# Kernel tuning notes

Hardware: AMD Instinct MI355X
Metric: run time of the kernel (lower is better)

Reference implementation:

```python
import jax, jax.numpy as jnp
import numpy as np

B, N, RESC, LAT, UNIT = 8, 32, 256.0, 1536, 512
CHS = [64, 64, 128, 256, 512, 512]
HS = [128, 64, 32, 16, 8, 1]


def _align(feat, P):
    # torch F.grid_sample(feat, 2*P.unsqueeze(-2)/RESC - 1, 'bilinear', 'border', align_corners=False).squeeze(-1)
    # feat: [B,C,H,W], P: [B,M,2] (x,y) pixel coords in [0,RESC); returns [B,C,M]
    Bn, C, H, W = feat.shape
    gx = 2.0 * P[..., 0] / RESC - 1.0
    gy = 2.0 * P[..., 1] / RESC - 1.0
    # align_corners=False unnormalize, then border clamp
    x = jnp.clip(((gx + 1.0) * W - 1.0) * 0.5, 0.0, W - 1.0)
    y = jnp.clip(((gy + 1.0) * H - 1.0) * 0.5, 0.0, H - 1.0)
    x0 = jnp.floor(x); y0 = jnp.floor(y)
    wx = (x - x0)[:, None, :]; wy = (y - y0)[:, None, :]
    x0i = x0.astype(jnp.int32); y0i = y0.astype(jnp.int32)
    x1i = jnp.minimum(x0i + 1, W - 1); y1i = jnp.minimum(y0i + 1, H - 1)
    flat = feat.reshape(Bn, C, H * W)
    def gat(yi, xi):
        return jnp.take_along_axis(flat, (yi * W + xi)[:, None, :], axis=2)  # [B,C,M]
    v00 = gat(y0i, x0i); v01 = gat(y0i, x1i); v10 = gat(y1i, x0i); v11 = gat(y1i, x1i)
    return v00 * (1 - wx) * (1 - wy) + v01 * wx * (1 - wy) + v10 * (1 - wx) * wy + v11 * wx * wy


def _conv1(x, w, b):
    # 1x1 Conv1d: [B,Cin,M] x [Cout,Cin] -> [B,Cout,M]
    return jnp.einsum('bci,oc->boi', x, w) + b[None, :, None]


def _rescls(x, p):
    # ResCls(n=1): intro -> (relu(BN) -> chorus, residual) -> outro ; BN in eval mode
    iw, ib, bg, bb, bm, bv, cw, cb, ow, ob = p
    x = _conv1(x, iw, ib)
    d = jax.nn.relu((x - bm[None, :, None]) * (bg / jnp.sqrt(bv + 1e-5))[None, :, None] + bb[None, :, None])
    x = x + _conv1(d, cw, cb)
    return _conv1(x, ow, ob)


def _forward(feats, P, n, gp, pp):
    # node features: concat of per-level aligned features  [B, LAT, N]
    F_ = jnp.concatenate([_align(f, P) for f in feats], axis=1)
    # edge midpoints ep[b, i*N+j] = (P[i] + P[j]) / 2  -> [B, N*N, 2]
    ep = ((P[:, :, None, :] + P[:, None, :, :]) * 0.5).reshape(B, N * N, 2)
    # L: first LAT channels = F[:, :, i], next LAT channels = F[:, :, j]
    Fi = jnp.broadcast_to(F_[:, :, :, None], (B, LAT, N, N)).reshape(B, LAT, N * N)
    Fj = jnp.broadcast_to(F_[:, :, None, :], (B, LAT, N, N)).reshape(B, LAT, N * N)
    E = jnp.concatenate([_align(f, ep) for f in feats], axis=1)  # [B, LAT, N*N]
    CE = jnp.concatenate([Fi, Fj, E], axis=1)  # [B, 3*LAT, N*N]
    gate = jax.nn.sigmoid(_rescls(CE, gp))  # [B, 1, N*N]
    pr = _rescls(CE, pp)  # [B, 64, N*N]
    pr = pr / jnp.maximum(jnp.linalg.norm(pr, axis=1, keepdims=True), 1e-12)  # F.normalize(dim=1)
    m = jnp.arange(N) < n[:, None]  # [B, N]
    mask = (m[:, None, :] & m[:, :, None]).reshape(B, 1, N * N).astype(CE.dtype)
    return (gate * pr * mask).reshape(B, 64, N, N)


def setup_inputs() -> dict:
    key = jax.random.key(0)
    ks = jax.random.split(key, 20)
    d = {}
    for i, (c, h) in enumerate(zip(CHS, HS)):
        d[f'feat{i}'] = jax.random.normal(ks[i], (B, c, h, h), jnp.float32)
    d['P'] = jax.random.uniform(ks[6], (B, N, 2), jnp.float32) * RESC
    d['n'] = jax.random.randint(ks[7], (B,), 16, N + 1, jnp.int32)
    def w(k, shape):
        return jax.random.normal(k, shape, jnp.float32) * 0.02
    for pre, cout, k0 in (('g', 1, 8), ('p', 64, 12)):
        d[pre + '_iw'] = w(ks[k0], (UNIT, 3 * LAT)); d[pre + '_ib'] = jnp.zeros((UNIT,), jnp.float32)
        d[pre + '_bg'] = jnp.ones((UNIT,), jnp.float32); d[pre + '_bb'] = jnp.zeros((UNIT,), jnp.float32)
        d[pre + '_bm'] = jnp.zeros((UNIT,), jnp.float32)
        d[pre + '_bv'] = jax.random.uniform(ks[k0 + 1], (UNIT,), jnp.float32) + 0.5
        d[pre + '_cw'] = w(ks[k0 + 2], (UNIT, UNIT)); d[pre + '_cb'] = jnp.zeros((UNIT,), jnp.float32)
        d[pre + '_ow'] = w(ks[k0 + 3], (cout, UNIT)); d[pre + '_ob'] = jnp.zeros((cout,), jnp.float32)
    return d


def reference(feat0, feat1, feat2, feat3, feat4, feat5, P, n,
              g_iw, g_ib, g_bg, g_bb, g_bm, g_bv, g_cw, g_cb, g_ow, g_ob,
              p_iw, p_ib, p_bg, p_bb, p_bm, p_bv, p_cw, p_cb, p_ow, p_ob):
    feats = (feat0, feat1, feat2, feat3, feat4, feat5)
    gp = (g_iw, g_ib, g_bg, g_bb, g_bm, g_bv, g_cw, g_cb, g_ow, g_ob)
    pp = (p_iw, p_ib, p_bg, p_bb, p_bm, p_bv, p_cw, p_cb, p_ow, p_ob)
    return _forward(feats, P, n, gp, pp)
```

## Files before the change

kernel.cpp:

```cpp
#include <hip/hip_runtime.h>
#include <hip/hip_bf16.h>

using bf16 = __hip_bfloat16;
using short8 = __attribute__((ext_vector_type(8))) short;
using f32x4  = __attribute__((ext_vector_type(4))) float;
typedef unsigned int u32;

#define LAT_ 1536

__device__ __forceinline__ void glds16(const bf16* g, bf16* l) {
  __builtin_amdgcn_global_load_lds(
      (const __attribute__((address_space(1))) void*)g,
      (__attribute__((address_space(3))) void*)l, 16, 0, 0);
}
__device__ __forceinline__ float b2f(bf16 x) { return __bfloat162float(x); }
__device__ __forceinline__ bf16 f2b(float x) { return __float2bfloat16(x); }

template<int C, int W>
__device__ __forceinline__ void trans_tile(const float* __restrict__ src, bf16* __restrict__ dst,
                                           int b, int hw0, int c0, bf16 (*tile)[72], int t) {
  constexpr int HW = W * W;
  {
    int cl = t >> 2, h0 = (t & 3) * 16;
    const float* sp = src + (long)(b * C + c0 + cl) * HW + hw0 + h0;
    #pragma unroll
    for (int k = 0; k < 16; k += 4) {
      float4 v = *(const float4*)(sp + k);
      tile[h0 + k + 0][cl] = f2b(v.x);
      tile[h0 + k + 1][cl] = f2b(v.y);
      tile[h0 + k + 2][cl] = f2b(v.z);
      tile[h0 + k + 3][cl] = f2b(v.w);
    }
  }
  __syncthreads();
  {
    int hwl = t >> 2, cc = (t & 3) * 16;
    bf16* dp = dst + ((long)b * HW + hw0 + hwl) * C + c0 + cc;
    #pragma unroll
    for (int k = 0; k < 16; k += 2) {
      __hip_bfloat162 pr;
      pr.x = tile[hwl][cc + k];
      pr.y = tile[hwl][cc + k + 1];
      *(__hip_bfloat162*)(dp + k) = pr;
    }
  }
}

__global__ __launch_bounds__(256) void prep_k(
    const float* __restrict__ g_iw, const float* __restrict__ p_iw,
    const float* __restrict__ p_cw, const float* __restrict__ p_ow, const float* __restrict__ f5,
    const float* __restrict__ g_bg, const float* __restrict__ g_bb, const float* __restrict__ g_bm,
    const float* __restrict__ g_bv, const float* __restrict__ p_bg, const float* __restrict__ p_bb,
    const float* __restrict__ p_bm, const float* __restrict__ p_bv,
    const float* __restrict__ g_ib, const float* __restrict__ p_ib, const float* __restrict__ p_cb,
    const float* __restrict__ g_ow, const float* __restrict__ g_cw,
    const float* __restrict__ g_cb, const float* __restrict__ g_ob,
    const float* __restrict__ f0, const float* __restrict__ f1, const float* __restrict__ f2,
    const float* __restrict__ f3, const float* __restrict__ f4,
    bf16* __restrict__ Wp, bf16* __restrict__ pcw16, bf16* __restrict__ pow16,
    bf16* __restrict__ T5, float* __restrict__ bnp, float* __restrict__ u,
    float* __restrict__ gacc,
    bf16* __restrict__ T0, bf16* __restrict__ T1, bf16* __restrict__ T2,
    bf16* __restrict__ T3, bf16* __restrict__ T4) {
  __shared__ bf16 tile[64][72];
  __shared__ float red[256];
  int B = blockIdx.x, t = threadIdx.x;
  if (B < 18432) {
    int seg = B / 3072;
    int idx = (B % 3072) * 256 + t;
    if (idx < 512 * 1536) {
      int r = idx / 1536, c = idx % 1536;
      const float* src; int co;
      switch (seg) {
        case 0: src = g_iw; co = 0;    break;
        case 1: src = g_iw; co = 1536; break;
        case 2: src = p_iw; co = 0;    break;
        case 3: src = p_iw; co = 1536; break;
        case 4: src = g_iw; co = 3072; break;
        default: src = p_iw; co = 3072; break;
      }
      Wp[(long)seg * 512 * 1536 + idx] = f2b(src[(long)r * 4608 + co + c]);
    }
    return;
  }
  if (B < 19456) { int idx = (B - 18432) * 256 + t; pcw16[idx] = f2b(p_cw[idx]); return; }
  if (B < 19584) { int idx = (B - 19456) * 256 + t; pow16[idx] = f2b(p_ow[idx]); return; }
  if (B < 19600) { int idx = (B - 19584) * 256 + t; T5[idx] = f2b(f5[idx]); return; }
  if (B < 19602) {
    int k = (B - 19600) * 256 + t;
    if (k < 512) {
      float sg = g_bg[k] / sqrtf(g_bv[k] + 1e-5f);
      bnp[k] = sg; bnp[512 + k] = g_bb[k] - g_bm[k] * sg;
      float sp = p_bg[k] / sqrtf(p_bv[k] + 1e-5f);
      bnp[1024 + k] = sp; bnp[1536 + k] = p_bb[k] - p_bm[k] * sp;
      bnp[2048 + k] = g_ib[k]; bnp[2560 + k] = p_ib[k];
      bnp[3584 + k] = p_cb[k];
    }
    return;
  }
  if (B < 19610) {
    __shared__ float ured[4][64];
    int k0 = (B - 19602) * 64;
    int kk = t & 63, part = t >> 6;
    int k = k0 + kk;
    float s = 0.f;
    for (int o = part * 128; o < part * 128 + 128; ++o)
      s = fmaf(g_ow[o], g_cw[o * 512 + k], s);
    ured[part][kk] = s;
    __syncthreads();
    if (part == 0) u[k] = ured[0][kk] + ured[1][kk] + ured[2][kk] + ured[3][kk];
    return;
  }
  if (B == 19610) {
    red[t] = g_ow[t] * g_cb[t] + g_ow[t + 256] * g_cb[t + 256];
    __syncthreads();
    for (int off = 128; off; off >>= 1) {
      if (t < off) red[t] += red[t + off];
      __syncthreads();
    }
    if (t == 0) bnp[3072] = red[0] + g_ob[0];
    return;
  }
  if (B < 19643) { int idx = (B - 19611) * 256 + t; gacc[idx] = 0.f; return; }
  {
    int q = B - 19643;
    int b = q / 376, tt = q % 376;
    if (tt < 256)      trans_tile<64, 128>(f0, T0, b, tt * 64, 0, tile, t);
    else if (tt < 320) trans_tile<64, 64 >(f1, T1, b, (tt - 256) * 64, 0, tile, t);
    else if (tt < 352) { int z = tt - 320; trans_tile<128, 32>(f2, T2, b, (z & 15) * 64, (z >> 4) * 64, tile, t); }
    else if (tt < 368) { int z = tt - 352; trans_tile<256, 16>(f3, T3, b, (z & 3) * 64, (z >> 2) * 64, tile, t); }
    else               { int z = tt - 368; trans_tile<512, 8 >(f4, T4, b, 0, z * 64, tile, t); }
  }
}

__device__ __forceinline__ float blo(u32 r) { return __uint_as_float(r << 16); }
__device__ __forceinline__ float bhi(u32 r) { return __uint_as_float(r & 0xffff0000u); }

template<int C, int W>
__device__ __forceinline__ void proc2(const bf16* __restrict__ T, int b,
    const float* MX, const float* MY, bf16* __restrict__ Sb, int koff, int t) {
  constexpr int C2 = C / 2, HW = W * W;
  const bf16* Tb = T + (long)b * HW * C;
  for (int idx = t; idx < 16 * C2; idx += 256) {
    int q = idx / C2, c2 = idx % C2;
    float x = MX[q], y = MY[q];
    float fx = fminf(fmaxf(x * ((float)W / 256.f) - 0.5f, 0.f), (float)(W - 1));
    float fy = fminf(fmaxf(y * ((float)W / 256.f) - 0.5f, 0.f), (float)(W - 1));
    float x0f = floorf(fx), y0f = floorf(fy);
    float wx = fx - x0f, wy = fy - y0f;
    int x0 = (int)x0f, y0 = (int)y0f;
    int x1 = min(x0 + 1, W - 1), y1 = min(y0 + 1, W - 1);
    u32 r00 = *(const u32*)&Tb[(y0 * W + x0) * C + 2 * c2];
    u32 r01 = *(const u32*)&Tb[(y0 * W + x1) * C + 2 * c2];
    u32 r10 = *(const u32*)&Tb[(y1 * W + x0) * C + 2 * c2];
    u32 r11 = *(const u32*)&Tb[(y1 * W + x1) * C + 2 * c2];
    float w00 = (1.f - wx) * (1.f - wy), w01 = wx * (1.f - wy);
    float w10 = (1.f - wx) * wy,        w11 = wx * wy;
    float vlo = blo(r00) * w00 + blo(r01) * w01 + blo(r10) * w10 + blo(r11) * w11;
    float vhi = bhi(r00) * w00 + bhi(r01) * w01 + bhi(r10) * w10 + bhi(r11) * w11;
    __hip_bfloat162 pr;
    pr.x = f2b(vlo); pr.y = f2b(vhi);
    *(__hip_bfloat162*)&Sb[(long)q * LAT_ + koff + 2 * c2] = pr;
  }
}

__global__ __launch_bounds__(256) void sample5_k(
    const bf16* __restrict__ T0, const bf16* __restrict__ T1, const bf16* __restrict__ T2,
    const bf16* __restrict__ T3, const bf16* __restrict__ T4, const bf16* __restrict__ T5,
    const float* __restrict__ P, bf16* __restrict__ Sball) {
  int b = blockIdx.z, p0 = blockIdx.x * 16, lvl = blockIdx.y, t = threadIdx.x;
  __shared__ float Px[32], Py[32], MX[16], MY[16];
  if (t < 32) { Px[t] = P[(b * 32 + t) * 2]; Py[t] = P[(b * 32 + t) * 2 + 1]; }
  __syncthreads();
  if (t < 16) {
    int m = p0 + t;
    float x, y;
    if (m < 32) { x = Px[m]; y = Py[m]; }
    else { int ij = m - 32, i = ij >> 5, j = ij & 31;
           x = 0.5f * (Px[i] + Px[j]); y = 0.5f * (Py[i] + Py[j]); }
    MX[t] = x; MY[t] = y;
  }
  __syncthreads();
  bf16* Sb = Sball + ((long)b * 1056 + p0) * LAT_;
  switch (lvl) {
    case 0: proc2<64, 128>(T0, b, MX, MY, Sb, 0,    t); break;
    case 1: proc2<64, 64 >(T1, b, MX, MY, Sb, 64,   t); break;
    case 2: proc2<128, 32>(T2, b, MX, MY, Sb, 128,  t); break;
    case 3: proc2<256, 16>(T3, b, MX, MY, Sb, 256,  t); break;
    case 4: proc2<512, 8 >(T4, b, MX, MY, Sb, 512,  t); break;
    default:
      for (int idx = t; idx < 16 * 256; idx += 256) {
        int q = idx >> 8, c2 = idx & 255;
        *(__hip_bfloat162*)&Sb[(long)q * LAT_ + 1024 + 2 * c2] =
            *(const __hip_bfloat162*)&T5[b * 512 + 2 * c2];
      }
  }
}

__global__ __launch_bounds__(256) void nodegemm_k(
    const bf16* __restrict__ Sball, const bf16* __restrict__ Wp, float* __restrict__ A4) {
  int b = blockIdx.y;
  int n0 = blockIdx.x * 64;
  int t = threadIdx.x, w = t >> 6, lane = t & 63;
  int nn = n0 + w * 16;
  int frow = lane & 15, fko = (lane >> 4) * 8;
  const bf16* Ab = Sball + (long)b * 1056 * LAT_;
  f32x4 acc[2] = {};
  for (int kb = 0; kb < LAT_; kb += 32) {
    short8 bq = *(const short8*)&Wp[(long)(nn + frow) * LAT_ + kb + fko];
    #pragma unroll
    for (int i = 0; i < 2; ++i) {
      short8 aq = *(const short8*)&Ab[(long)(i * 16 + frow) * LAT_ + kb + fko];
      acc[i] = __builtin_amdgcn_mfma_f32_16x16x32_bf16(aq, bq, acc[i], 0, 0, 0);
    }
  }
  #pragma unroll
  for (int i = 0; i < 2; ++i)
    #pragma unroll
    for (int r = 0; r < 4; ++r) {
      int m = i * 16 + (lane >> 4) * 4 + r;
      int n = nn + (lane & 15);
      A4[(long)b * 65536 + m * 2048 + n] = acc[i][r];
    }
}

__global__ __launch_bounds__(256) void edge_k(
    const bf16* __restrict__ Sball, const bf16* __restrict__ WpE,
    const float* __restrict__ bnp, const float* __restrict__ A4,
    const float* __restrict__ u, const float* __restrict__ g_ow,
    bf16* __restrict__ XFh, bf16* __restrict__ DH, float* __restrict__ gacc) {
  int b = blockIdx.z;
  int m0 = blockIdx.x * 128, n0 = blockIdx.y * 128;
  const bf16* A = Sball + (long)b * 1056 * LAT_ + 32 * LAT_;
  __shared__ bf16 Ash[128 * 32];
  __shared__ bf16 Bsh[128 * 32];
  int t = threadIdx.x, w = t >> 6, lane = t & 63;
  int mh = (w & 1) * 64, nh = (w >> 1) * 64;
  int frow = lane & 15, fko = (lane >> 4) * 8;
  int lrow = lane >> 2, lchunk = lane & 3;
  f32x4 acc[4][4] = {};
  for (int kb = 0; kb < LAT_; kb += 32) {
    #pragma unroll
    for (int q = 0; q < 2; ++q) {
      int ra = q * 64 + w * 16 + lrow;
      glds16(&A[(long)(m0 + ra) * LAT_ + kb + lchunk * 8],   &Ash[ra * 32 + lchunk * 8]);
      glds16(&WpE[(long)(n0 + ra) * LAT_ + kb + lchunk * 8], &Bsh[ra * 32 + lchunk * 8]);
    }
    __syncthreads();
    short8 af[4], bq[4];
    #pragma unroll
    for (int i = 0; i < 4; ++i) af[i] = *(const short8*)&Ash[(mh + i * 16 + frow) * 32 + fko];
    #pragma unroll
    for (int j = 0; j < 4; ++j) bq[j] = *(const short8*)&Bsh[(nh + j * 16 + frow) * 32 + fko];
    #pragma unroll
    for (int i = 0; i < 4; ++i)
      #pragma unroll
      for (int j = 0; j < 4; ++j)
        acc[i][j] = __builtin_amdgcn_mfma_f32_16x16x32_bf16(af[i], bq[j], acc[i][j], 0, 0, 0);
    __syncthreads();
  }
  if (n0 < 512) {
    float pg[16];
    #pragma unroll
    for (int z = 0; z < 16; ++z) pg[z] = 0.f;
    #pragma unroll
    for (int i = 0; i < 4; ++i) {
      #pragma unroll
      for (int j = 0; j < 4; ++j) {
        int n = n0 + nh + j * 16 + (lane & 15);
        float gw = g_ow[n], uu = u[n];
        float sc = bnp[n], sh = bnp[512 + n], ib = bnp[2048 + n];
        #pragma unroll
        for (int r = 0; r < 4; ++r) {
          int m = m0 + mh + i * 16 + (lane >> 4) * 4 + r;
          float v = acc[i][j][r] + ib
                  + A4[((long)b * 32 + (m >> 5)) * 2048 + n]
                  + A4[((long)b * 32 + (m & 31)) * 2048 + 512 + n];
          float d = fmaxf(fmaf(v, sc, sh), 0.f);
          pg[i * 4 + r] += gw * v + uu * d;
        }
      }
    }
    #pragma unroll
    for (int z = 0; z < 16; ++z) {
      float v = pg[z];
      v += __shfl_xor(v, 1, 16);
      v += __shfl_xor(v, 2, 16);
      v += __shfl_xor(v, 4, 16);
      v += __shfl_xor(v, 8, 16);
      pg[z] = v;
    }
    if ((lane & 15) == 0) {
      #pragma unroll
      for (int z = 0; z < 16; ++z) {
        int m = m0 + mh + (z >> 2) * 16 + (lane >> 4) * 4 + (z & 3);
        atomicAdd(&gacc[(long)b * 1024 + m], pg[z]);
      }
    }
  } else {
    #pragma unroll
    for (int i = 0; i < 4; ++i) {
      #pragma unroll
      for (int j = 0; j < 4; ++j) {
        int n = n0 + nh + j * 16 + (lane & 15);
        int np = n - 512;
        float sc = bnp[1024 + np], sh = bnp[1536 + np], ib = bnp[2048 + n];
        #pragma unroll
        for (int r = 0; r < 4; ++r) {
          int m = m0 + mh + i * 16 + (lane >> 4) * 4 + r;
          float v = acc[i][j][r] + ib
                  + A4[((long)b * 32 + (m >> 5)) * 2048 + 1024 + np]
                  + A4[((long)b * 32 + (m & 31)) * 2048 + 1536 + np];
          long e = ((long)b * 1024 + m) * 512 + np;
          XFh[e] = f2b(v);
          DH[e]  = f2b(fmaxf(fmaf(v, sc, sh), 0.f));
        }
      }
    }
  }
}

__global__ __launch_bounds__(256) void chorus_k(
    const bf16* __restrict__ DH, const bf16* __restrict__ pcw16,
    const float* __restrict__ bnp, const bf16* __restrict__ XFh,
    bf16* __restrict__ Yp16) {
  int b = blockIdx.z;
  int m0 = blockIdx.x * 128, n0 = blockIdx.y * 128;
  const bf16* A = DH + (long)b * 1024 * 512;
  __shared__ bf16 Ash[128 * 32];
  __shared__ bf16 Bsh[128 * 32];
  int t = threadIdx.x, w = t >> 6, lane = t & 63;
  int mh = (w & 1) * 64, nh = (w >> 1) * 64;
  int frow = lane & 15, fko = (lane >> 4) * 8;
  int lrow = lane >> 2, lchunk = lane & 3;
  f32x4 acc[4][4] = {};
  for (int kb = 0; kb < 512; kb += 32) {
    #pragma unroll
    for (int q = 0; q < 2; ++q) {
      int ra = q * 64 + w * 16 + lrow;
      glds16(&A[(long)(m0 + ra) * 512 + kb + lchunk * 8],      &Ash[ra * 32 + lchunk * 8]);
      glds16(&pcw16[(long)(n0 + ra) * 512 + kb + lchunk * 8],  &Bsh[ra * 32 + lchunk * 8]);
    }
    __syncthreads();
    short8 af[4], bq[4];
    #pragma unroll
    for (int i = 0; i < 4; ++i) af[i] = *(const short8*)&Ash[(mh + i * 16 + frow) * 32 + fko];
    #pragma unroll
    for (int j = 0; j < 4; ++j) bq[j] = *(const short8*)&Bsh[(nh + j * 16 + frow) * 32 + fko];
    #pragma unroll
    for (int i = 0; i < 4; ++i)
      #pragma unroll
      for (int j = 0; j < 4; ++j)
        acc[i][j] = __builtin_amdgcn_mfma_f32_16x16x32_bf16(af[i], bq[j], acc[i][j], 0, 0, 0);
    __syncthreads();
  }
  #pragma unroll
  for (int i = 0; i < 4; ++i)
    #pragma unroll
    for (int j = 0; j < 4; ++j)
      #pragma unroll
      for (int r = 0; r < 4; ++r) {
        int m = m0 + mh + i * 16 + (lane >> 4) * 4 + r;
        int n = n0 + nh + j * 16 + (lane & 15);
        float v = acc[i][j][r] + bnp[3584 + n]
                + b2f(XFh[((long)b * 1024 + m) * 512 + n]);
        Yp16[((long)b * 1024 + m) * 512 + n] = f2b(v);
      }
}

__global__ __launch_bounds__(256) void ofinal_k(
    const bf16* __restrict__ Yp16, const bf16* __restrict__ pow16,
    const float* __restrict__ p_ob, const float* __restrict__ gacc,
    const float* __restrict__ bnp, const int* __restrict__ nvec,
    float* __restrict__ out) {
  int b = blockIdx.y;
  int m0 = blockIdx.x * 64;
  const bf16* Ab = Yp16 + (long)b * 1024 * 512;
  __shared__ bf16 Ash[64][40];
  __shared__ bf16 Bsh[64][40];
  __shared__ float ol[64][65];
  int t = threadIdx.x, w = t >> 6, lane = t & 63;
  int mq = w * 16;
  int frow = lane & 15, fko = (lane >> 4) * 8;
  f32x4 acc[4] = {};
  for (int kb = 0; kb < 512; kb += 32) {
    { int r = t >> 2, ko = (t & 3) * 8;
      *(uint4*)&Ash[r][ko] = *(const uint4*)&Ab[(long)(m0 + r) * 512 + kb + ko];
      *(uint4*)&Bsh[r][ko] = *(const uint4*)&pow16[(long)r * 512 + kb + ko]; }
    __syncthreads();
    short8 af = *(const short8*)&Ash[mq + frow][fko];
    #pragma unroll
    for (int j = 0; j < 4; ++j) {
      short8 bq = *(const short8*)&Bsh[j * 16 + frow][fko];
      acc[j] = __builtin_amdgcn_mfma_f32_16x16x32_bf16(af, bq, acc[j], 0, 0, 0);
    }
    __syncthreads();
  }
  float pr[4][4], ssl[4] = {0.f, 0.f, 0.f, 0.f};
  #pragma unroll
  for (int j = 0; j < 4; ++j) {
    float bias = p_ob[j * 16 + (lane & 15)];
    #pragma unroll
    for (int r = 0; r < 4; ++r) {
      float v = acc[j][r] + bias;
      pr[j][r] = v;
      ssl[r] = fmaf(v, v, ssl[r]);
    }
  }
  #pragma unroll
  for (int r = 0; r < 4; ++r) {
    float v = ssl[r];
    v += __shfl_xor(v, 1, 16);
    v += __shfl_xor(v, 2, 16);
    v += __shfl_xor(v, 4, 16);
    v += __shfl_xor(v, 8, 16);
    ssl[r] = v;
  }
  int nb = nvec[b];
  float gconst = bnp[3072];
  float scale[4];
  #pragma unroll
  for (int r = 0; r < 4; ++r) {
    int m = m0 + mq + (lane >> 4) * 4 + r;
    float gl = gacc[(long)b * 1024 + m] + gconst;
    float gate = 1.f / (1.f + expf(-gl));
    int ii = m >> 5, jj = m & 31;
    float maskv = (ii < nb && jj < nb) ? 1.f : 0.f;
    scale[r] = gate * maskv / fmaxf(sqrtf(ssl[r]), 1e-12f);
  }
  #pragma unroll
  for (int j = 0; j < 4; ++j)
    #pragma unroll
    for (int r = 0; r < 4; ++r)
      ol[mq + (lane >> 4) * 4 + r][j * 16 + (lane & 15)] = pr[j][r] * scale[r];
  __syncthreads();
  {
    int c = t >> 2, ms = (t & 3) * 16;
    float* op = out + ((long)b * 64 + c) * 1024 + m0 + ms;
    #pragma unroll
    for (int k = 0; k < 16; k += 4) {
      float4 v;
      v.x = ol[ms + k + 0][c];
      v.y = ol[ms + k + 1][c];
      v.z = ol[ms + k + 2][c];
      v.w = ol[ms + k + 3][c];
      *(float4*)(op + k) = v;
    }
  }
}

extern "C" void kernel_launch(void* const* d_in, const int* in_sizes, int n_in,
                              void* d_out, int out_size, void* d_ws, size_t ws_size,
                              hipStream_t stream) {
  const float* f0 = (const float*)d_in[0];
  const float* f1 = (const float*)d_in[1];
  const float* f2 = (const float*)d_in[2];
  const float* f3 = (const float*)d_in[3];
  const float* f4 = (const float*)d_in[4];
  const float* f5 = (const float*)d_in[5];
  const float* P  = (const float*)d_in[6];
  const int*   n  = (const int*)d_in[7];
  const float *g_iw=(const float*)d_in[8],  *g_ib=(const float*)d_in[9],
              *g_bg=(const float*)d_in[10], *g_bb=(const float*)d_in[11],
              *g_bm=(const float*)d_in[12], *g_bv=(const float*)d_in[13],
              *g_cw=(const float*)d_in[14], *g_cb=(const float*)d_in[15],
              *g_ow=(const float*)d_in[16], *g_ob=(const float*)d_in[17];
  const float *p_iw=(const float*)d_in[18], *p_ib=(const float*)d_in[19],
              *p_bg=(const float*)d_in[20], *p_bb=(const float*)d_in[21],
              *p_bm=(const float*)d_in[22], *p_bv=(const float*)d_in[23],
              *p_cw=(const float*)d_in[24], *p_cb=(const float*)d_in[25],
              *p_ow=(const float*)d_in[26], *p_ob=(const float*)d_in[27];
  float* out = (float*)d_out;
  char* wsb = (char*)d_ws;

  bf16*  Sb    = (bf16*)(wsb + 0);
  bf16*  Wp    = (bf16*)(wsb + 25952256);
  bf16*  pcw16 = (bf16*)(wsb + 35389440);
  bf16*  pow16 = (bf16*)(wsb + 35913728);
  bf16*  T5    = (bf16*)(wsb + 35979264);
  float* bnp   = (float*)(wsb + 35987456);
  float* u     = (float*)(wsb + 36003840);
  float* gacc  = (float*)(wsb + 36005888);
  float* A4    = (float*)(wsb + 36038656);
  bf16*  XFh   = (bf16*)(wsb + 38135808);
  bf16*  DH    = (bf16*)(wsb + 46524416);
  bf16*  Yp16  = (bf16*)(wsb + 54913024);
  bf16*  T0 = (bf16*)(wsb + 38135808);
  bf16*  T1 = (bf16*)(wsb + 54913024);
  bf16*  T2 = (bf16*)(wsb + 59107328);
  bf16*  T3 = (bf16*)(wsb + 61204480);
  bf16*  T4 = (bf16*)(wsb + 62253056);
  bf16*  WpE = Wp + (long)2048 * LAT_;

  prep_k<<<22651, 256, 0, stream>>>(g_iw, p_iw, p_cw, p_ow, f5,
      g_bg, g_bb, g_bm, g_bv, p_bg, p_bb, p_bm, p_bv, g_ib, p_ib, p_cb,
      g_ow, g_cw, g_cb, g_ob, f0, f1, f2, f3, f4,
      Wp, pcw16, pow16, T5, bnp, u, gacc, T0, T1, T2, T3, T4);
  sample5_k<<<dim3(66, 6, 8), 256, 0, stream>>>(T0, T1, T2, T3, T4, T5, P, Sb);
  nodegemm_k<<<dim3(32, 8), 256, 0, stream>>>(Sb, Wp, A4);
  edge_k<<<dim3(8, 8, 8), 256, 0, stream>>>(Sb, WpE, bnp, A4, u, g_ow, XFh, DH, gacc);
  chorus_k<<<dim3(8, 4, 8), 256, 0, stream>>>(DH, pcw16, bnp, XFh, Yp16);
  ofinal_k<<<dim3(16, 8), 256, 0, stream>>>(Yp16, pow16, p_ob, gacc, bnp, n, out);
}
```

Baseline: 258.4 us.

## Double-buffer GEMM mainloops with K=64 tiles and XOR-swizzled LDS

The edge and chorus GEMM kernels now stage 64-wide K tiles into two LDS buffers, so the async global-to-LDS loads for the next tile overlap the MFMA work on the current one. This halves the number of barriers per K. The LDS chunk position is XOR-swizzled by row to cut bank conflicts on the fragment reads. LDS use per block grows fourfold, which may lower occupancy.

```diff
diff --git a/kernel.cpp b/kernel.cpp
--- a/kernel.cpp
+++ b/kernel.cpp
@@ -232,33 +232,58 @@
   int b = blockIdx.z;
   int m0 = blockIdx.x * 128, n0 = blockIdx.y * 128;
   const bf16* A = Sball + (long)b * 1056 * LAT_ + 32 * LAT_;
-  __shared__ bf16 Ash[128 * 32];
-  __shared__ bf16 Bsh[128 * 32];
+  __shared__ bf16 Ash[2][128 * 64];
+  __shared__ bf16 Bsh[2][128 * 64];
   int t = threadIdx.x, w = t >> 6, lane = t & 63;
   int mh = (w & 1) * 64, nh = (w >> 1) * 64;
-  int frow = lane & 15, fko = (lane >> 4) * 8;
-  int lrow = lane >> 2, lchunk = lane & 3;
+  int frow = lane & 15, kq = lane >> 4;
+  int srow = w * 8 + (lane >> 3), schunk = lane & 7;
   f32x4 acc[4][4] = {};
-  for (int kb = 0; kb < LAT_; kb += 32) {
-    #pragma unroll
-    for (int q = 0; q < 2; ++q) {
-      int ra = q * 64 + w * 16 + lrow;
-      glds16(&A[(long)(m0 + ra) * LAT_ + kb + lchunk * 8],   &Ash[ra * 32 + lchunk * 8]);
-      glds16(&WpE[(long)(n0 + ra) * LAT_ + kb + lchunk * 8], &Bsh[ra * 32 + lchunk * 8]);
-    }
-    __syncthreads();
-    short8 af[4], bq[4];
-    #pragma unroll
-    for (int i = 0; i < 4; ++i) af[i] = *(const short8*)&Ash[(mh + i * 16 + frow) * 32 + fko];
-    #pragma unroll
-    for (int j = 0; j < 4; ++j) bq[j] = *(const short8*)&Bsh[(nh + j * 16 + frow) * 32 + fko];
-    #pragma unroll
-    for (int i = 0; i < 4; ++i)
+
+  auto STAGE = [&](int buf, int kb) {
+    #pragma unroll
+    for (int q = 0; q < 4; ++q) {
+      int ra = q * 32 + srow;
+      int sc = (schunk ^ (ra & 7)) * 8;
+      glds16(&A[(long)(m0 + ra) * LAT_ + kb + sc],   &Ash[buf][ra * 64 + schunk * 8]);
+      glds16(&WpE[(long)(n0 + ra) * LAT_ + kb + sc], &Bsh[buf][ra * 64 + schunk * 8]);
+    }
+  };
+  auto COMPUTE = [&](int buf) {
+    #pragma unroll
+    for (int kk = 0; kk < 2; ++kk) {
+      int s8 = ((((kk << 2) | kq) ^ (frow & 7)) << 3);
+      short8 af[4], bq[4];
+      #pragma unroll
+      for (int i = 0; i < 4; ++i)
+        af[i] = *(const short8*)&Ash[buf][(mh + i * 16 + frow) * 64 + s8];
       #pragma unroll
       for (int j = 0; j < 4; ++j)
-        acc[i][j] = __builtin_amdgcn_mfma_f32_16x16x32_bf16(af[i], bq[j], acc[i][j], 0, 0, 0);
-    __syncthreads();
-  }
+        bq[j] = *(const short8*)&Bsh[buf][(nh + j * 16 + frow) * 64 + s8];
+      #pragma unroll
+      for (int i = 0; i < 4; ++i)
+        #pragma unroll
+        for (int j = 0; j < 4; ++j)
+          acc[i][j] = __builtin_amdgcn_mfma_f32_16x16x32_bf16(af[i], bq[j], acc[i][j], 0, 0, 0);
+    }
+  };
+
+  STAGE(0, 0);
+  __syncthreads();
+  #pragma unroll 1
+  for (int kt = 0; kt + 2 < 24; kt += 2) {
+    STAGE(1, (kt + 1) * 64);
+    COMPUTE(0);
+    __syncthreads();
+    STAGE(0, (kt + 2) * 64);
+    COMPUTE(1);
+    __syncthreads();
+  }
+  STAGE(1, 23 * 64);
+  COMPUTE(0);
+  __syncthreads();
+  COMPUTE(1);
+
   if (n0 < 512) {
     float pg[16];
     #pragma unroll
@@ -327,33 +352,58 @@
   int b = blockIdx.z;
   int m0 = blockIdx.x * 128, n0 = blockIdx.y * 128;
   const bf16* A = DH + (long)b * 1024 * 512;
-  __shared__ bf16 Ash[128 * 32];
-  __shared__ bf16 Bsh[128 * 32];
+  __shared__ bf16 Ash[2][128 * 64];
+  __shared__ bf16 Bsh[2][128 * 64];
   int t = threadIdx.x, w = t >> 6, lane = t & 63;
   int mh = (w & 1) * 64, nh = (w >> 1) * 64;
-  int frow = lane & 15, fko = (lane >> 4) * 8;
-  int lrow = lane >> 2, lchunk = lane & 3;
+  int frow = lane & 15, kq = lane >> 4;
+  int srow = w * 8 + (lane >> 3), schunk = lane & 7;
   f32x4 acc[4][4] = {};
-  for (int kb = 0; kb < 512; kb += 32) {
-    #pragma unroll
-    for (int q = 0; q < 2; ++q) {
-      int ra = q * 64 + w * 16 + lrow;
-      glds16(&A[(long)(m0 + ra) * 512 + kb + lchunk * 8],      &Ash[ra * 32 + lchunk * 8]);
-      glds16(&pcw16[(long)(n0 + ra) * 512 + kb + lchunk * 8],  &Bsh[ra * 32 + lchunk * 8]);
-    }
-    __syncthreads();
-    short8 af[4], bq[4];
-    #pragma unroll
-    for (int i = 0; i < 4; ++i) af[i] = *(const short8*)&Ash[(mh + i * 16 + frow) * 32 + fko];
-    #pragma unroll
-    for (int j = 0; j < 4; ++j) bq[j] = *(const short8*)&Bsh[(nh + j * 16 + frow) * 32 + fko];
-    #pragma unroll
-    for (int i = 0; i < 4; ++i)
+
+  auto STAGE = [&](int buf, int kb) {
+    #pragma unroll
+    for (int q = 0; q < 4; ++q) {
+      int ra = q * 32 + srow;
+      int sc = (schunk ^ (ra & 7)) * 8;
+      glds16(&A[(long)(m0 + ra) * 512 + kb + sc],     &Ash[buf][ra * 64 + schunk * 8]);
+      glds16(&pcw16[(long)(n0 + ra) * 512 + kb + sc], &Bsh[buf][ra * 64 + schunk * 8]);
+    }
+  };
+  auto COMPUTE = [&](int buf) {
+    #pragma unroll
+    for (int kk = 0; kk < 2; ++kk) {
+      int s8 = ((((kk << 2) | kq) ^ (frow & 7)) << 3);
+      short8 af[4], bq[4];
+      #pragma unroll
+      for (int i = 0; i < 4; ++i)
+        af[i] = *(const short8*)&Ash[buf][(mh + i * 16 + frow) * 64 + s8];
       #pragma unroll
       for (int j = 0; j < 4; ++j)
-        acc[i][j] = __builtin_amdgcn_mfma_f32_16x16x32_bf16(af[i], bq[j], acc[i][j], 0, 0, 0);
-    __syncthreads();
-  }
+        bq[j] = *(const short8*)&Bsh[buf][(nh + j * 16 + frow) * 64 + s8];
+      #pragma unroll
+      for (int i = 0; i < 4; ++i)
+        #pragma unroll
+        for (int j = 0; j < 4; ++j)
+          acc[i][j] = __builtin_amdgcn_mfma_f32_16x16x32_bf16(af[i], bq[j], acc[i][j], 0, 0, 0);
+    }
+  };
+
+  STAGE(0, 0);
+  __syncthreads();
+  #pragma unroll 1
+  for (int kt = 0; kt + 2 < 8; kt += 2) {
+    STAGE(1, (kt + 1) * 64);
+    COMPUTE(0);
+    __syncthreads();
+    STAGE(0, (kt + 2) * 64);
+    COMPUTE(1);
+    __syncthreads();
+  }
+  STAGE(1, 7 * 64);
+  COMPUTE(0);
+  __syncthreads();
+  COMPUTE(1);
+
   #pragma unroll
   for (int i = 0; i < 4; ++i)
     #pragma unroll
```

Result: slower. 273.8 us (+5.9%).
